# Optimization experiments

Measured on AMD Instinct MI355X. Metric: run time of the kernel, lower is better.

Reference implementation:

```python
import jax, jax.numpy as jnp
import numpy as np


def setup_inputs() -> dict:
    key = jax.random.key(0)
    k1, k2 = jax.random.split(key)
    N, C, H, W = 2, 128, 256, 256
    k, m = 7, 8
    feat = jax.random.normal(k1, (N, C, H, W), dtype=jnp.float32)
    filters_lr = jax.random.normal(k2, (N, C * k * k, H // m, W // m), dtype=jnp.float32)
    return {"feat": feat, "filters_lr": filters_lr, "kernel_size": k, "block_size": m}


def _block_fac(feat, filters_lr, k, m):
    # feat: [N,C,H,W]; filters_lr: [N, C*k^2, H/m, W/m]
    N, C, H, W = feat.shape
    Hb, Wb = H // m, W // m
    k2 = k * k
    pad = (k - 1) // 2
    # weight_permute_reshape: NCHW -> NHWC -> [N,Hb,Wb,C,k2] (C slowest, then tap)
    w = jnp.transpose(filters_lr, (0, 2, 3, 1)).reshape(N, Hb, Wb, C, k2)
    x = jnp.transpose(feat, (0, 2, 3, 1))  # NHWC
    xp = jnp.pad(x, ((0, 0), (pad, pad), (pad, pad), (0, 0)))
    out = jnp.zeros_like(x)
    # tap index t = dh*k + dw (matches torch unfold(2,k) then unfold(3,k) ordering)
    for t in range(k2):
        dh, dw = t // k, t % k
        # per-block weight for this tap, upsampled to full resolution: [N,H,W,C]
        w_t = jnp.repeat(jnp.repeat(w[..., t], m, axis=1), m, axis=2)
        out = out + xp[:, dh:dh + H, dw:dw + W, :] * w_t
    return jnp.transpose(out, (0, 3, 1, 2))  # back to NCHW


def reference(feat, filters_lr, kernel_size, block_size):
    return _block_fac(feat, filters_lr, kernel_size, block_size)
```

## Files before the change

kernel.cpp:

```cpp
#include <hip/hip_runtime.h>


__global__ __launch_bounds__(256, 1)
void block_fac_kernel(const float* __restrict__ feat,
                      const float* __restrict__ filt,
                      float* __restrict__ out) {
    const int wid = (blockIdx.x << 2) | (threadIdx.x >> 6);
    const int hb  = wid & 31;
    const int c   = (wid >> 5) & 127;
    const int n   = wid >> 12;
    const int lane = threadIdx.x & 63;

    const int c0 = lane << 2;
    const int wb = lane >> 1;
    const int H0 = hb * 8;

    const float* fbase  = feat + (size_t)(n * 128 + c) * (256 * 256);
    const float* wgbase = filt + (size_t)((n * 128 + c) * 49) * 1024 + hb * 32 + wb;

    float4 row[14];
    #pragma unroll
    for (int r = 0; r < 14; ++r) {
        int gr  = H0 - 3 + r;
        int grc = gr < 0 ? 0 : (gr > 255 ? 255 : gr);
        row[r] = *(const float4*)(fbase + (size_t)grc * 256 + c0);
    }

    float wt[49];
    #pragma unroll
    for (int t = 0; t < 49; ++t) wt[t] = wgbase[(size_t)t * 1024];

    const int addrL = ((lane - 1) & 63) << 2;
    const int addrR = ((lane + 1) & 63) << 2;
    const bool l0  = (lane == 0);
    const bool l63 = (lane == 63);

    float acc[8][4] = {};

    #pragma unroll
    for (int jj = 0; jj < 14; ++jj) {
        const int gr = H0 - 3 + jj;
        float4 f = row[jj];
        if (gr < 0 || gr > 255) f = make_float4(0.f, 0.f, 0.f, 0.f);

        float L1 = __int_as_float(__builtin_amdgcn_ds_bpermute(addrL, __float_as_int(f.y)));
        float L2 = __int_as_float(__builtin_amdgcn_ds_bpermute(addrL, __float_as_int(f.z)));
        float L3 = __int_as_float(__builtin_amdgcn_ds_bpermute(addrL, __float_as_int(f.w)));
        float R0 = __int_as_float(__builtin_amdgcn_ds_bpermute(addrR, __float_as_int(f.x)));
        float R1 = __int_as_float(__builtin_amdgcn_ds_bpermute(addrR, __float_as_int(f.y)));
        float R2 = __int_as_float(__builtin_amdgcn_ds_bpermute(addrR, __float_as_int(f.z)));
        if (l0)  { L1 = 0.f; L2 = 0.f; L3 = 0.f; }
        if (l63) { R0 = 0.f; R1 = 0.f; R2 = 0.f; }

        float win[12] = {0.f, L1, L2, L3,
                         f.x, f.y, f.z, f.w,
                         R0, R1, R2, 0.f};
        #pragma unroll
        for (int a = 0; a < 8; ++a) {
            int dh = jj - a;
            if (dh >= 0 && dh <= 6) {
                #pragma unroll
                for (int dw = 0; dw < 7; ++dw) {
                    float wv = wt[dh * 7 + dw];
                    #pragma unroll
                    for (int i = 0; i < 4; ++i)
                        acc[a][i] += win[i + dw + 1] * wv;
                }
            }
        }
    }

    float* obase = out + (size_t)((n * 128 + c) * 256 + H0) * 256 + c0;
    #pragma unroll
    for (int a = 0; a < 8; ++a)
        *(float4*)(obase + (size_t)(a * 256)) =
            make_float4(acc[a][0], acc[a][1], acc[a][2], acc[a][3]);
}

extern "C" void kernel_launch(void* const* d_in, const int* in_sizes, int n_in,
                              void* d_out, int out_size, void* d_ws, size_t ws_size,
                              hipStream_t stream) {
    const float* feat = (const float*)d_in[0];
    const float* filt = (const float*)d_in[1];
    float* out = (float*)d_out;
    dim3 grid(2 * 128 * 32 / 4);
    dim3 block(256);
    hipLaunchKernelGGL(block_fac_kernel, grid, block, 0, stream, feat, filt, out);
}
```

Measured before the change: 40.70 us.

## Stage per-block filter weights via LDS async loads, widen blocks, nontemporal stores

Blocks grow to 8 waves that cover 8 consecutive block-rows of one channel. The 49 filter taps for those rows are copied cooperatively into LDS with global_load_lds, as coalesced 16-byte loads, replacing strided 4-byte scalar global loads per lane. Each wave then reads its weights from LDS after a barrier. Output stores become nontemporal to avoid polluting the cache. This adds a block-wide sync and LDS traffic, and halves the number of blocks.

```diff
diff --git a/kernel.cpp b/kernel.cpp
--- a/kernel.cpp
+++ b/kernel.cpp
@@ -1,22 +1,39 @@
 #include <hip/hip_runtime.h>
+#include <stdint.h>
 
 
-__global__ __launch_bounds__(256, 1)
+#define NW 8
+
+typedef const uint32_t __attribute__((address_space(1))) guint;
+typedef uint32_t __attribute__((address_space(3))) luint;
+typedef float __attribute__((ext_vector_type(4))) fx4;
+
+__global__ __launch_bounds__(512, 1)
 void block_fac_kernel(const float* __restrict__ feat,
                       const float* __restrict__ filt,
                       float* __restrict__ out) {
-    const int wid = (blockIdx.x << 2) | (threadIdx.x >> 6);
-    const int hb  = wid & 31;
-    const int c   = (wid >> 5) & 127;
-    const int n   = wid >> 12;
+    __shared__ float s_w[49 * 8 * 32];
+
+    const int bid  = blockIdx.x;
+    const int g    = bid & 3;
+    const int c    = (bid >> 2) & 127;
+    const int n    = bid >> 9;
+    const int wave = threadIdx.x >> 6;
     const int lane = threadIdx.x & 63;
 
+    const int hb = g * 8 + wave;
+    const int H0 = hb * 8;
     const int c0 = lane << 2;
     const int wb = lane >> 1;
-    const int H0 = hb * 8;
 
-    const float* fbase  = feat + (size_t)(n * 128 + c) * (256 * 256);
-    const float* wgbase = filt + (size_t)((n * 128 + c) * 49) * 1024 + hb * 32 + wb;
+    const float* fbase  = feat + (size_t)(n * 128 + c) * 65536;
+    const float* wtbase = filt + (size_t)((n * 128 + c) * 49) * 1024 + g * 256;
+
+    for (int t = wave; t < 49; t += NW) {
+        const float* gp = wtbase + (size_t)t * 1024 + (lane << 2);
+        float* lp = s_w + t * 256;
+        __builtin_amdgcn_global_load_lds((guint*)gp, (luint*)lp, 16, 0, 0);
+    }
 
     float4 row[14];
     #pragma unroll
@@ -26,9 +43,12 @@
         row[r] = *(const float4*)(fbase + (size_t)grc * 256 + c0);
     }
 
+    __syncthreads();
+
+    const float* ws = s_w + wave * 32 + wb;
     float wt[49];
     #pragma unroll
-    for (int t = 0; t < 49; ++t) wt[t] = wgbase[(size_t)t * 1024];
+    for (int t = 0; t < 49; ++t) wt[t] = ws[t * 256];
 
     const int addrL = ((lane - 1) & 63) << 2;
     const int addrR = ((lane + 1) & 63) << 2;
@@ -72,9 +92,10 @@
 
     float* obase = out + (size_t)((n * 128 + c) * 256 + H0) * 256 + c0;
     #pragma unroll
-    for (int a = 0; a < 8; ++a)
-        *(float4*)(obase + (size_t)(a * 256)) =
-            make_float4(acc[a][0], acc[a][1], acc[a][2], acc[a][3]);
+    for (int a = 0; a < 8; ++a) {
+        fx4 v = {acc[a][0], acc[a][1], acc[a][2], acc[a][3]};
+        __builtin_nontemporal_store(v, (fx4*)(obase + (size_t)(a * 256)));
+    }
 }
 
 extern "C" void kernel_launch(void* const* d_in, const int* in_sizes, int n_in,
@@ -83,7 +104,7 @@
     const float* feat = (const float*)d_in[0];
     const float* filt = (const float*)d_in[1];
     float* out = (float*)d_out;
-    dim3 grid(2 * 128 * 32 / 4);
-    dim3 block(256);
+    dim3 grid(2 * 128 * 4);
+    dim3 block(512);
     hipLaunchKernelGGL(block_fac_kernel, grid, block, 0, stream, feat, filt, out);
 }
```

Measured after the change: 80.64 us. 98.1% more time.

## Process four row-blocks per wave with double-buffered LDS weight staging

Applied to the files above, without the earlier changes.

Each wave now loops over four consecutive 8-row blocks instead of one. Filter taps for the next block are staged into per-wave LDS slabs through global_load_lds, and the next block's feature rows are prefetched into registers while the current block is computed, with explicit vmcnt waits. The grid shrinks to 512 blocks, so latency hiding shifts from many waves to software pipelining within each wave. This costs extra register pressure from a second row buffer and adds a hand-tuned waitcnt that must match the issued load count.

```diff
diff --git a/kernel.cpp b/kernel.cpp
--- a/kernel.cpp
+++ b/kernel.cpp
@@ -1,80 +1,130 @@
 #include <hip/hip_runtime.h>
+#include <stdint.h>
 
+
+#define SLABF 1568
+
+typedef const uint32_t __attribute__((address_space(1))) guint;
+typedef uint32_t __attribute__((address_space(3))) luint;
+
+#define STAGE_W(WT, DST)                                                        \
+  do {                                                                          \
+    _Pragma("unroll") for (int i_ = 0; i_ < 7; ++i_)                            \
+      if (i_ < 6 || lane < 8) {                                                 \
+        int f_ = (i_ << 6) | lane;                                              \
+        __builtin_amdgcn_global_load_lds(                                       \
+            (guint*)((WT) + (size_t)(f_ >> 3) * 1024 + (f_ & 7) * 4),           \
+            (luint*)((DST) + i_ * 256), 16, 0, 0);                              \
+      }                                                                         \
+  } while (0)
+
+#define LOAD_ROWS(H0v, DST)                                                     \
+  do {                                                                          \
+    _Pragma("unroll") for (int r_ = 0; r_ < 14; ++r_) {                         \
+      int gr_  = (H0v) - 3 + r_;                                                \
+      int grc_ = gr_ < 0 ? 0 : (gr_ > 255 ? 255 : gr_);                         \
+      (DST)[r_] = *(const float4*)(fbase + (size_t)grc_ * 256 + c0);            \
+    }                                                                           \
+  } while (0)
 
 __global__ __launch_bounds__(256, 1)
 void block_fac_kernel(const float* __restrict__ feat,
                       const float* __restrict__ filt,
                       float* __restrict__ out) {
-    const int wid = (blockIdx.x << 2) | (threadIdx.x >> 6);
-    const int hb  = wid & 31;
-    const int c   = (wid >> 5) & 127;
-    const int n   = wid >> 12;
+    __shared__ float s_w[4][2][SLABF];
+
+    const int wave = threadIdx.x >> 6;
     const int lane = threadIdx.x & 63;
+    const int wid  = (blockIdx.x << 2) | wave;
+    const int q    = wid & 7;
+    const int c    = (wid >> 3) & 127;
+    const int n    = wid >> 10;
 
     const int c0 = lane << 2;
     const int wb = lane >> 1;
-    const int H0 = hb * 8;
 
-    const float* fbase  = feat + (size_t)(n * 128 + c) * (256 * 256);
-    const float* wgbase = filt + (size_t)((n * 128 + c) * 49) * 1024 + hb * 32 + wb;
-
-    float4 row[14];
-    #pragma unroll
-    for (int r = 0; r < 14; ++r) {
-        int gr  = H0 - 3 + r;
-        int grc = gr < 0 ? 0 : (gr > 255 ? 255 : gr);
-        row[r] = *(const float4*)(fbase + (size_t)grc * 256 + c0);
-    }
-
-    float wt[49];
-    #pragma unroll
-    for (int t = 0; t < 49; ++t) wt[t] = wgbase[(size_t)t * 1024];
+    const float* fbase = feat + (size_t)(n * 128 + c) * 65536;
+    const float* wtapb = filt + (size_t)((n * 128 + c) * 49) * 1024;
+    float* slab0 = &s_w[wave][0][0];
+    float* slab1 = &s_w[wave][1][0];
 
     const int addrL = ((lane - 1) & 63) << 2;
     const int addrR = ((lane + 1) & 63) << 2;
     const bool l0  = (lane == 0);
     const bool l63 = (lane == 63);
 
-    float acc[8][4] = {};
+    float4 rowA[14], rowB[14];
 
-    #pragma unroll
-    for (int jj = 0; jj < 14; ++jj) {
-        const int gr = H0 - 3 + jj;
-        float4 f = row[jj];
-        if (gr < 0 || gr > 255) f = make_float4(0.f, 0.f, 0.f, 0.f);
+    STAGE_W(wtapb + (q * 4 + 0) * 32, slab0);
+    __builtin_amdgcn_sched_barrier(0);
+    LOAD_ROWS(q * 32, rowA);
+    __builtin_amdgcn_sched_barrier(0);
 
-        float L1 = __int_as_float(__builtin_amdgcn_ds_bpermute(addrL, __float_as_int(f.y)));
-        float L2 = __int_as_float(__builtin_amdgcn_ds_bpermute(addrL, __float_as_int(f.z)));
-        float L3 = __int_as_float(__builtin_amdgcn_ds_bpermute(addrL, __float_as_int(f.w)));
-        float R0 = __int_as_float(__builtin_amdgcn_ds_bpermute(addrR, __float_as_int(f.x)));
-        float R1 = __int_as_float(__builtin_amdgcn_ds_bpermute(addrR, __float_as_int(f.y)));
-        float R2 = __int_as_float(__builtin_amdgcn_ds_bpermute(addrR, __float_as_int(f.z)));
-        if (l0)  { L1 = 0.f; L2 = 0.f; L3 = 0.f; }
-        if (l63) { R0 = 0.f; R1 = 0.f; R2 = 0.f; }
+    #pragma unroll 1
+    for (int t = 0; t < 4; ++t) {
+        __builtin_amdgcn_sched_barrier(0);
+        asm volatile("s_waitcnt vmcnt(8)" ::: "memory");
+        __builtin_amdgcn_sched_barrier(0);
 
-        float win[12] = {0.f, L1, L2, L3,
-                         f.x, f.y, f.z, f.w,
-                         R0, R1, R2, 0.f};
+        const float* ws = (t & 1 ? slab1 : slab0) + wb;
+        float wt[49];
         #pragma unroll
-        for (int a = 0; a < 8; ++a) {
-            int dh = jj - a;
-            if (dh >= 0 && dh <= 6) {
-                #pragma unroll
-                for (int dw = 0; dw < 7; ++dw) {
-                    float wv = wt[dh * 7 + dw];
+        for (int k = 0; k < 49; ++k) wt[k] = ws[k * 32];
+
+        const int H0 = (q * 4 + t) * 8;
+
+        if (t < 3) {
+            STAGE_W(wtapb + (q * 4 + t + 1) * 32, (t & 1 ? slab0 : slab1));
+            __builtin_amdgcn_sched_barrier(0);
+            LOAD_ROWS(H0 + 8, rowB);
+            __builtin_amdgcn_sched_barrier(0);
+        }
+
+        float acc[8][4] = {};
+        #pragma unroll
+        for (int jj = 0; jj < 14; ++jj) {
+            const int gr = H0 - 3 + jj;
+            float4 f = rowA[jj];
+            if (gr < 0 || gr > 255) f = make_float4(0.f, 0.f, 0.f, 0.f);
+
+            float L1 = __int_as_float(__builtin_amdgcn_ds_bpermute(addrL, __float_as_int(f.y)));
+            float L2 = __int_as_float(__builtin_amdgcn_ds_bpermute(addrL, __float_as_int(f.z)));
+            float L3 = __int_as_float(__builtin_amdgcn_ds_bpermute(addrL, __float_as_int(f.w)));
+            float R0 = __int_as_float(__builtin_amdgcn_ds_bpermute(addrR, __float_as_int(f.x)));
+            float R1 = __int_as_float(__builtin_amdgcn_ds_bpermute(addrR, __float_as_int(f.y)));
+            float R2 = __int_as_float(__builtin_amdgcn_ds_bpermute(addrR, __float_as_int(f.z)));
+            if (l0)  { L1 = 0.f; L2 = 0.f; L3 = 0.f; }
+            if (l63) { R0 = 0.f; R1 = 0.f; R2 = 0.f; }
+
+            float win[12] = {0.f, L1, L2, L3,
+                             f.x, f.y, f.z, f.w,
+                             R0, R1, R2, 0.f};
+            #pragma unroll
+            for (int a = 0; a < 8; ++a) {
+                int dh = jj - a;
+                if (dh >= 0 && dh <= 6) {
                     #pragma unroll
-                    for (int i = 0; i < 4; ++i)
-                        acc[a][i] += win[i + dw + 1] * wv;
+                    for (int dw = 0; dw < 7; ++dw) {
+                        float wv = wt[dh * 7 + dw];
+                        #pragma unroll
+                        for (int i = 0; i < 4; ++i)
+                            acc[a][i] += win[i + dw + 1] * wv;
+                    }
                 }
             }
         }
+
+        float* obase = out + (size_t)((n * 128 + c) * 256 + H0) * 256 + c0;
+        #pragma unroll
+        for (int a = 0; a < 8; ++a)
+            *(float4*)(obase + (size_t)(a * 256)) =
+                make_float4(acc[a][0], acc[a][1], acc[a][2], acc[a][3]);
+
+        if (t < 3) {
+            #pragma unroll
+            for (int r = 0; r < 14; ++r) rowA[r] = rowB[r];
+        }
     }
-
-    float* obase = out + (size_t)((n * 128 + c) * 256 + H0) * 256 + c0;
-    #pragma unroll
-    for (int a = 0; a < 8; ++a)
-        *(float4*)(obase + (size_t)(a * 256)) =
-            make_float4(acc[a][0], acc[a][1], acc[a][2], acc[a][3]);
 }
 
 extern "C" void kernel_launch(void* const* d_in, const int* in_sizes, int n_in,
@@ -83,7 +133,7 @@
     const float* feat = (const float*)d_in[0];
     const float* filt = (const float*)d_in[1];
     float* out = (float*)d_out;
-    dim3 grid(2 * 128 * 32 / 4);
+    dim3 grid(512);
     dim3 block(256);
     hipLaunchKernelGGL(block_fac_kernel, grid, block, 0, stream, feat, filt, out);
 }
```

Result: slower. 49.03 us (+20.5%).
